# Optimization experiments

Hardware: AMD Instinct MI355X
Metric: run time of the kernel (lower is better)

## Reference

```python
import jax, jax.numpy as jnp
import numpy as np
import math

D_MODEL = 1024
NUM_HEADS = 16
HEAD_DIM = D_MODEL // NUM_HEADS


def _xavier(key, out_f, in_f):
    limit = math.sqrt(6.0 / (in_f + out_f))
    return jax.random.uniform(key, (out_f, in_f), jnp.float32, -limit, limit)


def ternarize(w):
    # abs-mean threshold -> {-1, 0, +1}
    abs_mean = jnp.mean(jnp.abs(w))
    return jnp.where(jnp.abs(w) > abs_mean, jnp.sign(w), jnp.zeros_like(w))


def setup_inputs() -> dict:
    key = jax.random.key(0)
    kq, kk, kv, kwq, kwk, kwv, kwo = jax.random.split(key, 7)
    B, S = 2, 2048
    return {
        "query": jax.random.normal(kq, (B, S, D_MODEL), jnp.float32),
        "key": jax.random.normal(kk, (B, S, D_MODEL), jnp.float32),
        "value": jax.random.normal(kv, (B, S, D_MODEL), jnp.float32),
        "w_q": _xavier(kwq, D_MODEL, D_MODEL),
        "w_k": _xavier(kwk, D_MODEL, D_MODEL),
        "w_v": _xavier(kwv, D_MODEL, D_MODEL),
        "w_o": _xavier(kwo, D_MODEL, D_MODEL),
    }


def reference(query, key, value, w_q, w_k, w_v, w_o):
    B, S, _ = query.shape
    # ternary projections (F.linear: x @ W.T)
    q = query @ ternarize(w_q).T
    k = key @ ternarize(w_k).T
    v = value @ ternarize(w_v).T
    # [B, H, S, Dh]
    q = q.reshape(B, S, NUM_HEADS, HEAD_DIM).transpose(0, 2, 1, 3)
    k = k.reshape(B, -1, NUM_HEADS, HEAD_DIM).transpose(0, 2, 1, 3)
    v = v.reshape(B, -1, NUM_HEADS, HEAD_DIM).transpose(0, 2, 1, 3)
    scores = jnp.einsum("bhqd,bhkd->bhqk", q, k) / math.sqrt(HEAD_DIM)
    probs = jax.nn.softmax(scores, axis=-1)
    out = jnp.einsum("bhqk,bhkd->bhqd", probs, v)
    out = out.transpose(0, 2, 1, 3).reshape(B, S, D_MODEL)
    return out @ ternarize(w_o).T
```

## Files before the change

kernel.cpp:

```cpp
#include <hip/hip_runtime.h>
#include <cstdint>
#include <cstddef>

typedef __bf16 bfloat;
typedef __bf16 bf16x8 __attribute__((ext_vector_type(8)));
typedef __bf16 bf16x4 __attribute__((ext_vector_type(4)));
typedef float  f32x4  __attribute__((ext_vector_type(4)));

static constexpr int D  = 1024;
static constexpr int S  = 2048;
static constexpr int B  = 2;
static constexpr int H  = 16;
static constexpr int DH = 64;
static constexpr int M  = B * S;
static constexpr int WMAT_N = 1024 * 1024;

#define MFMA_BF16(a, b, c) __builtin_amdgcn_mfma_f32_16x16x32_bf16((a), (b), (c), 0, 0, 0)

__device__ __forceinline__ void gl_lds16(const void* g, void* l) {
  __builtin_amdgcn_global_load_lds(
      (const __attribute__((address_space(1))) void*)g,
      (__attribute__((address_space(3))) void*)l, 16, 0, 0);
}

__global__ void absum_kernel(const float* __restrict__ w0, const float* __restrict__ w1,
                             const float* __restrict__ w2, const float* __restrict__ w3,
                             double* __restrict__ sums) {
  int z = blockIdx.y;
  const float* w = (z == 0) ? w0 : (z == 1) ? w1 : (z == 2) ? w2 : w3;
  const float4* w4 = (const float4*)w;
  double s = 0.0;
  for (int i = blockIdx.x * blockDim.x + threadIdx.x; i < (WMAT_N / 4);
       i += gridDim.x * blockDim.x) {
    float4 v = w4[i];
    s += (double)fabsf(v.x) + (double)fabsf(v.y) + (double)fabsf(v.z) + (double)fabsf(v.w);
  }
  for (int off = 1; off < 64; off <<= 1) s += __shfl_xor(s, off, 64);
  __shared__ double ps[4];
  if ((threadIdx.x & 63) == 0) ps[threadIdx.x >> 6] = s;
  __syncthreads();
  if (threadIdx.x == 0) atomicAdd(&sums[z], ps[0] + ps[1] + ps[2] + ps[3]);
}

__global__ void tern_kernel(const float* __restrict__ w0, const float* __restrict__ w1,
                            const float* __restrict__ w2, const float* __restrict__ w3,
                            bfloat* __restrict__ o0, bfloat* __restrict__ o1,
                            bfloat* __restrict__ o2, bfloat* __restrict__ o3,
                            const double* __restrict__ sums) {
  int z = blockIdx.y;
  const float* w = (z == 0) ? w0 : (z == 1) ? w1 : (z == 2) ? w2 : w3;
  bfloat* o = (z == 0) ? o0 : (z == 1) ? o1 : (z == 2) ? o2 : o3;
  double thr = sums[z] * (1.0 / (double)WMAT_N);
  const float4* w4 = (const float4*)w;
  for (int i = blockIdx.x * blockDim.x + threadIdx.x; i < (WMAT_N / 4);
       i += gridDim.x * blockDim.x) {
    float4 v = w4[i];
    bf16x4 r;
    r[0] = (bfloat)(((double)fabsf(v.x) > thr) ? (v.x > 0.f ? 1.f : -1.f) : 0.f);
    r[1] = (bfloat)(((double)fabsf(v.y) > thr) ? (v.y > 0.f ? 1.f : -1.f) : 0.f);
    r[2] = (bfloat)(((double)fabsf(v.z) > thr) ? (v.z > 0.f ? 1.f : -1.f) : 0.f);
    r[3] = (bfloat)(((double)fabsf(v.w) > thr) ? (v.w > 0.f ? 1.f : -1.f) : 0.f);
    *(bf16x4*)&o[(size_t)i * 4] = r;
  }
}

__global__ void splitcvt3_kernel(const float* __restrict__ qx, const float* __restrict__ kx,
                                 const float* __restrict__ vx, bfloat* __restrict__ qhi,
                                 bfloat* __restrict__ qlo, bfloat* __restrict__ khi,
                                 bfloat* __restrict__ klo, bfloat* __restrict__ vhi) {
  int z = blockIdx.y;
  const float* x = (z == 0) ? qx : (z == 1) ? kx : vx;
  bfloat* hi = (z == 0) ? qhi : (z == 1) ? khi : vhi;
  bfloat* lo = (z == 0) ? qlo : (z == 1) ? klo : nullptr;
  const int n4 = M * D / 4;
  const float4* x4 = (const float4*)x;
  for (int i = blockIdx.x * blockDim.x + threadIdx.x; i < n4; i += gridDim.x * blockDim.x) {
    float4 v = x4[i];
    bf16x4 h;
    h[0] = (bfloat)v.x; h[1] = (bfloat)v.y; h[2] = (bfloat)v.z; h[3] = (bfloat)v.w;
    *(bf16x4*)&hi[(size_t)i * 4] = h;
    if (z < 2) {
      bf16x4 l;
      l[0] = (bfloat)(v.x - (float)h[0]);
      l[1] = (bfloat)(v.y - (float)h[1]);
      l[2] = (bfloat)(v.z - (float)h[2]);
      l[3] = (bfloat)(v.w - (float)h[3]);
      *(bf16x4*)&lo[(size_t)i * 4] = l;
    }
  }
}

__global__ __launch_bounds__(256) void qkv_gemm(
    const bfloat* __restrict__ xqh, const bfloat* __restrict__ xql,
    const bfloat* __restrict__ xkh, const bfloat* __restrict__ xkl,
    const bfloat* __restrict__ xvh, const bfloat* __restrict__ wqt,
    const bfloat* __restrict__ wkt, const bfloat* __restrict__ wvt,
    bfloat* __restrict__ qmh, bfloat* __restrict__ qml,
    bfloat* __restrict__ kmh, bfloat* __restrict__ kml, bfloat* __restrict__ vtr) {
  constexpr int K = D;
  constexpr int N = D;
  __shared__ __align__(16) bfloat As0[128 * 32];
  __shared__ __align__(16) bfloat As1[128 * 32];
  __shared__ __align__(16) bfloat Ws[128 * 32];

  const int z = blockIdx.z;
  const bfloat *A0, *A1 = nullptr, *Wm;
  bfloat *Oh = nullptr, *Ol = nullptr;
  float scale = 1.f;
  bool split;
  if (z == 0) {
    A0 = xqh; A1 = xql; Wm = wqt; Oh = qmh; Ol = qml;
    scale = 0.18033688f;
    split = true;
  } else if (z == 1) {
    A0 = xkh; A1 = xkl; Wm = wkt; Oh = kmh; Ol = kml; split = true;
  } else {
    A0 = xvh; Wm = wvt; split = false;
  }

  const int t = threadIdx.x;
  const int w = t >> 6, lane = t & 63;
  const int quad = lane >> 4, l16 = lane & 15;
  const int wm = w >> 1, wn = w & 1;
  const int m0 = blockIdx.y * 128, n0 = blockIdx.x * 128;

  f32x4 acc[4][4] = {};

  const int sr = t >> 2;
  const int cp = t & 3;
  const int cla = cp ^ ((sr >> 1) & 3);
  const int clb = cp ^ (((sr + 64) >> 1) & 3);

  const bfloat* pA0a = A0 + (size_t)(m0 + sr) * K + cla * 8;
  const bfloat* pA0b = A0 + (size_t)(m0 + 64 + sr) * K + clb * 8;
  const bfloat* pA1a = split ? A1 + (size_t)(m0 + sr) * K + cla * 8 : nullptr;
  const bfloat* pA1b = split ? A1 + (size_t)(m0 + 64 + sr) * K + clb * 8 : nullptr;
  const bfloat* pWa = Wm + (size_t)(n0 + sr) * K + cla * 8;
  const bfloat* pWb = Wm + (size_t)(n0 + 64 + sr) * K + clb * 8;

  for (int kk = 0; kk < K; kk += 32) {
    gl_lds16(pA0a + kk, As0 + w * 512);
    gl_lds16(pA0b + kk, As0 + 2048 + w * 512);
    if (split) {
      gl_lds16(pA1a + kk, As1 + w * 512);
      gl_lds16(pA1b + kk, As1 + 2048 + w * 512);
    }
    gl_lds16(pWa + kk, Ws + w * 512);
    gl_lds16(pWb + kk, Ws + 2048 + w * 512);
    __syncthreads();

    bf16x8 bfrag[4], afrag[4];
#pragma unroll
    for (int nt = 0; nt < 4; nt++) {
      int r = wn * 64 + nt * 16 + l16;
      bfrag[nt] = *(const bf16x8*)&Ws[r * 32 + ((quad ^ ((r >> 1) & 3)) * 8)];
    }
#pragma unroll
    for (int mt = 0; mt < 4; mt++) {
      int r = wm * 64 + mt * 16 + l16;
      afrag[mt] = *(const bf16x8*)&As0[r * 32 + ((quad ^ ((r >> 1) & 3)) * 8)];
    }
#pragma unroll
    for (int mt = 0; mt < 4; mt++)
#pragma unroll
      for (int nt = 0; nt < 4; nt++)
        acc[mt][nt] = MFMA_BF16(afrag[mt], bfrag[nt], acc[mt][nt]);
    if (split) {
#pragma unroll
      for (int mt = 0; mt < 4; mt++) {
        int r = wm * 64 + mt * 16 + l16;
        afrag[mt] = *(const bf16x8*)&As1[r * 32 + ((quad ^ ((r >> 1) & 3)) * 8)];
      }
#pragma unroll
      for (int mt = 0; mt < 4; mt++)
#pragma unroll
        for (int nt = 0; nt < 4; nt++)
          acc[mt][nt] = MFMA_BF16(afrag[mt], bfrag[nt], acc[mt][nt]);
    }
    __syncthreads();
  }

#pragma unroll
  for (int mt = 0; mt < 4; mt++) {
#pragma unroll
    for (int nt = 0; nt < 4; nt++) {
      const int row = m0 + wm * 64 + mt * 16 + quad * 4;
      const int col = n0 + wn * 64 + nt * 16 + l16;
      if (split) {
#pragma unroll
        for (int rg = 0; rg < 4; rg++) {
          float vv = acc[mt][nt][rg] * scale;
          size_t idx = (size_t)(row + rg) * N + col;
          bfloat hh = (bfloat)vv;
          Oh[idx] = hh;
          Ol[idx] = (bfloat)(vv - (float)hh);
        }
      } else {
        int bb = row >> 11, s = row & (S - 1);
        bf16x4 pk;
#pragma unroll
        for (int rg = 0; rg < 4; rg++) pk[rg] = (bfloat)acc[mt][nt][rg];
        *(bf16x4*)&vtr[(size_t)bb * D * S + (size_t)col * S + s] = pk;
      }
    }
  }
}

__global__ __launch_bounds__(256) void gemm_wo(const bfloat* __restrict__ A,
                                               const bfloat* __restrict__ Wm,
                                               float* __restrict__ Cf) {
  constexpr int K = D;
  constexpr int N = D;
  __shared__ __align__(16) bfloat As[128 * 32];
  __shared__ __align__(16) bfloat Ws[64 * 32];

  const int t = threadIdx.x;
  const int w = t >> 6, lane = t & 63;
  const int quad = lane >> 4, l16 = lane & 15;
  const int wm = w >> 1, wn = w & 1;
  const int m0 = blockIdx.y * 128, n0 = blockIdx.x * 64;

  f32x4 acc[4][2] = {};

  const int sr = t >> 2;
  const int cp = t & 3;
  const int cla = cp ^ ((sr >> 1) & 3);
  const int clb = cp ^ (((sr + 64) >> 1) & 3);
  const bfloat* pAa = A + (size_t)(m0 + sr) * K + cla * 8;
  const bfloat* pAb = A + (size_t)(m0 + 64 + sr) * K + clb * 8;
  const bfloat* pW = Wm + (size_t)(n0 + sr) * K + cla * 8;

  for (int kk = 0; kk < K; kk += 32) {
    gl_lds16(pAa + kk, As + w * 512);
    gl_lds16(pAb + kk, As + 2048 + w * 512);
    gl_lds16(pW + kk, Ws + w * 512);
    __syncthreads();

    bf16x8 bfrag[2], afrag[4];
#pragma unroll
    for (int nt = 0; nt < 2; nt++) {
      int r = wn * 32 + nt * 16 + l16;
      bfrag[nt] = *(const bf16x8*)&Ws[r * 32 + ((quad ^ ((r >> 1) & 3)) * 8)];
    }
#pragma unroll
    for (int mt = 0; mt < 4; mt++) {
      int r = wm * 64 + mt * 16 + l16;
      afrag[mt] = *(const bf16x8*)&As[r * 32 + ((quad ^ ((r >> 1) & 3)) * 8)];
    }
#pragma unroll
    for (int mt = 0; mt < 4; mt++)
#pragma unroll
      for (int nt = 0; nt < 2; nt++)
        acc[mt][nt] = MFMA_BF16(afrag[mt], bfrag[nt], acc[mt][nt]);
    __syncthreads();
  }

#pragma unroll
  for (int mt = 0; mt < 4; mt++) {
#pragma unroll
    for (int nt = 0; nt < 2; nt++) {
      const int row = m0 + wm * 64 + mt * 16 + quad * 4;
      const int col = n0 + wn * 32 + nt * 16 + l16;
#pragma unroll
      for (int rg = 0; rg < 4; rg++) Cf[(size_t)(row + rg) * N + col] = acc[mt][nt][rg];
    }
  }
}

__global__ __launch_bounds__(256) void flash_kernel(
    const bfloat* __restrict__ qh, const bfloat* __restrict__ ql,
    const bfloat* __restrict__ kh, const bfloat* __restrict__ kl,
    const bfloat* __restrict__ vt, bfloat* __restrict__ outp) {
  __shared__ __align__(16) bfloat Kh[64 * 64];
  __shared__ __align__(16) bfloat Kl[64 * 64];
  __shared__ __align__(16) bfloat Vt[64 * 64];
  __shared__ __align__(16) bfloat Pm[64 * 64];

  const int t = threadIdx.x;
  const int w = t >> 6, lane = t & 63;
  const int quad = lane >> 4, l16 = lane & 15;
  const int b = blockIdx.z, h = blockIdx.y;
  const int q0 = blockIdx.x * 64;
  const size_t base = (size_t)b * S * D + (size_t)h * DH;
  const size_t vbase = (size_t)b * D * S + (size_t)h * DH * S;

  const int ssr = lane >> 3;
  const int spc = lane & 7;

  bf16x8 ones;
#pragma unroll
  for (int j = 0; j < 8; j++) ones[j] = (bfloat)1.f;

#pragma unroll
  for (int g = 0; g < 2; g++) {
    int r = w * 16 + g * 8 + ssr;
    int c = spc ^ (r & 7);
    int lo = (w * 16 + g * 8) * 64;
    gl_lds16(qh + base + (size_t)(q0 + r) * D + c * 8, Kh + lo);
    gl_lds16(ql + base + (size_t)(q0 + r) * D + c * 8, Kl + lo);
  }
  __syncthreads();
  bf16x8 qhf[2], qlf[2];
  {
    int row = w * 16 + l16;
#pragma unroll
    for (int s2 = 0; s2 < 2; s2++) {
      qhf[s2] = *(const bf16x8*)&Kh[row * 64 + (((s2 * 4 + quad) ^ (l16 & 7)) * 8)];
      qlf[s2] = *(const bf16x8*)&Kl[row * 64 + (((s2 * 4 + quad) ^ (l16 & 7)) * 8)];
    }
  }
  __syncthreads();

  f32x4 Oa[4] = {};
  f32x4 La = {};
  float m_i = -3.0e38f;

  for (int k0 = 0; k0 < S; k0 += 64) {
#pragma unroll
    for (int g = 0; g < 2; g++) {
      int r = w * 16 + g * 8 + ssr;
      int c = spc ^ (r & 7);
      int lo = (w * 16 + g * 8) * 64;
      gl_lds16(kh + base + (size_t)(k0 + r) * D + c * 8, Kh + lo);
      gl_lds16(kl + base + (size_t)(k0 + r) * D + c * 8, Kl + lo);
      gl_lds16(vt + vbase + (size_t)r * S + k0 + c * 8, Vt + lo);
    }
    __syncthreads();

    f32x4 sf[4];
#pragma unroll
    for (int mt = 0; mt < 4; mt++) {
      f32x4 a = {};
      int krow = mt * 16 + l16;
#pragma unroll
      for (int s2 = 0; s2 < 2; s2++) {
        bf16x8 bh = *(const bf16x8*)&Kh[krow * 64 + (((s2 * 4 + quad) ^ (l16 & 7)) * 8)];
        bf16x8 bl = *(const bf16x8*)&Kl[krow * 64 + (((s2 * 4 + quad) ^ (l16 & 7)) * 8)];
        a = MFMA_BF16(bh, qhf[s2], a);
        a = MFMA_BF16(bl, qhf[s2], a);
        a = MFMA_BF16(bh, qlf[s2], a);
      }
      sf[mt] = a;
    }

    float mm = sf[0][0];
#pragma unroll
    for (int mt = 0; mt < 4; mt++)
#pragma unroll
      for (int rg = 0; rg < 4; rg++) mm = fmaxf(mm, sf[mt][rg]);
    mm = fmaxf(mm, __shfl_xor(mm, 16, 64));
    mm = fmaxf(mm, __shfl_xor(mm, 32, 64));
    if (__ballot(mm > m_i)) {
      float mnew = fmaxf(m_i, mm);
      float alpha = exp2f(m_i - mnew);
      m_i = mnew;
#pragma unroll
      for (int mt = 0; mt < 4; mt++) Oa[mt] *= alpha;
      La *= alpha;
    }
#pragma unroll
    for (int mt = 0; mt < 4; mt++)
#pragma unroll
      for (int rg = 0; rg < 4; rg++) sf[mt][rg] = exp2f(sf[mt][rg] - m_i);

#pragma unroll
    for (int mt = 0; mt < 4; mt++) {
      bf16x4 pk;
#pragma unroll
      for (int rg = 0; rg < 4; rg++) pk[rg] = (bfloat)sf[mt][rg];
      int g16 = (mt * 2 + (quad >> 1)) ^ (l16 & 7);
      *(bf16x4*)&Pm[(w * 16 + l16) * 64 + g16 * 8 + (quad & 1) * 4] = pk;
    }

#pragma unroll
    for (int s2 = 0; s2 < 2; s2++) {
      bf16x8 pb = *(const bf16x8*)&Pm[(w * 16 + l16) * 64 +
                                      (((s2 * 4 + quad) ^ (l16 & 7)) * 8)];
#pragma unroll
      for (int mt = 0; mt < 4; mt++) {
        int vrow = mt * 16 + l16;
        bf16x8 va = *(const bf16x8*)&Vt[vrow * 64 + (((s2 * 4 + quad) ^ (l16 & 7)) * 8)];
        Oa[mt] = MFMA_BF16(va, pb, Oa[mt]);
      }
      La = MFMA_BF16(ones, pb, La);
    }
    __syncthreads();
  }

  float inv = 1.0f / La[0];
  const int qrow = q0 + w * 16 + l16;
#pragma unroll
  for (int mt = 0; mt < 4; mt++) {
    bf16x4 ov;
#pragma unroll
    for (int rg = 0; rg < 4; rg++) ov[rg] = (bfloat)(Oa[mt][rg] * inv);
    *(bf16x4*)&outp[base + (size_t)qrow * D + mt * 16 + quad * 4] = ov;
  }
}

extern "C" void kernel_launch(void* const* d_in, const int* in_sizes, int n_in,
                              void* d_out, int out_size, void* d_ws, size_t ws_size,
                              hipStream_t stream) {
  const float* q_in = (const float*)d_in[0];
  const float* k_in = (const float*)d_in[1];
  const float* v_in = (const float*)d_in[2];
  const float* wq = (const float*)d_in[3];
  const float* wk = (const float*)d_in[4];
  const float* wv = (const float*)d_in[5];
  const float* wo = (const float*)d_in[6];
  float* outp = (float*)d_out;
  char* ws = (char*)d_ws;

  constexpr size_t WBYTES = (size_t)WMAT_N * 2;
  constexpr size_t XBYTES = (size_t)M * D * 2;
  size_t off = 0;
  double* sums = (double*)(ws + off); off += 256;
  bfloat* wqt = (bfloat*)(ws + off); off += WBYTES;
  bfloat* wkt = (bfloat*)(ws + off); off += WBYTES;
  bfloat* wvt = (bfloat*)(ws + off); off += WBYTES;
  bfloat* wot = (bfloat*)(ws + off); off += WBYTES;
  bfloat* xqh = (bfloat*)(ws + off); off += XBYTES;
  bfloat* xql = (bfloat*)(ws + off); off += XBYTES;
  bfloat* xkh = (bfloat*)(ws + off); off += XBYTES;
  bfloat* xkl = (bfloat*)(ws + off); off += XBYTES;
  bfloat* xvh = (bfloat*)(ws + off); off += XBYTES;
  bfloat* qmh = (bfloat*)(ws + off); off += XBYTES;
  bfloat* qml = (bfloat*)(ws + off); off += XBYTES;
  bfloat* kmh = (bfloat*)(ws + off); off += XBYTES;
  bfloat* kml = (bfloat*)(ws + off); off += XBYTES;
  bfloat* vtr = (bfloat*)(ws + off); off += XBYTES;
  bfloat* attn = xqh;

  hipMemsetAsync(sums, 0, 4 * sizeof(double), stream);
  absum_kernel<<<dim3(128, 4), 256, 0, stream>>>(wq, wk, wv, wo, sums);
  tern_kernel<<<dim3(128, 4), 256, 0, stream>>>(wq, wk, wv, wo, wqt, wkt, wvt, wot, sums);
  splitcvt3_kernel<<<dim3(512, 3), 256, 0, stream>>>(q_in, k_in, v_in, xqh, xql, xkh, xkl, xvh);
  qkv_gemm<<<dim3(D / 128, M / 128, 3), 256, 0, stream>>>(
      xqh, xql, xkh, xkl, xvh, wqt, wkt, wvt, qmh, qml, kmh, kml, vtr);
  flash_kernel<<<dim3(S / 64, H, B), 256, 0, stream>>>(qmh, qml, kmh, kml, vtr, attn);
  gemm_wo<<<dim3(D / 64, M / 128), 256, 0, stream>>>(attn, wot, outp);
}
```

Baseline: 299.4 us.

## Merge prep kernels, deepen QKV GEMM K-tile, shrink output GEMM tiles

Folds the weight abs-sum reduction and the fp32-to-bf16 split conversion into one launch, and widens the conversion to 8 elements per thread. The QKV GEMM now stages 64-wide K slices with an XOR swizzle, which halves the number of barrier round trips per tile. The output projection GEMM moves to 64x64 tiles with a launch-bounds hint, giving more blocks for a small problem. The costs are a larger LDS footprint in the QKV GEMM, which may lower occupancy, and less reuse per block in the output GEMM.

```diff
diff --git a/kernel.cpp b/kernel.cpp
--- a/kernel.cpp
+++ b/kernel.cpp
@@ -23,23 +23,51 @@
       (__attribute__((address_space(3))) void*)l, 16, 0, 0);
 }
 
-__global__ void absum_kernel(const float* __restrict__ w0, const float* __restrict__ w1,
-                             const float* __restrict__ w2, const float* __restrict__ w3,
-                             double* __restrict__ sums) {
-  int z = blockIdx.y;
-  const float* w = (z == 0) ? w0 : (z == 1) ? w1 : (z == 2) ? w2 : w3;
-  const float4* w4 = (const float4*)w;
-  double s = 0.0;
-  for (int i = blockIdx.x * blockDim.x + threadIdx.x; i < (WMAT_N / 4);
-       i += gridDim.x * blockDim.x) {
-    float4 v = w4[i];
-    s += (double)fabsf(v.x) + (double)fabsf(v.y) + (double)fabsf(v.z) + (double)fabsf(v.w);
-  }
-  for (int off = 1; off < 64; off <<= 1) s += __shfl_xor(s, off, 64);
-  __shared__ double ps[4];
-  if ((threadIdx.x & 63) == 0) ps[threadIdx.x >> 6] = s;
-  __syncthreads();
-  if (threadIdx.x == 0) atomicAdd(&sums[z], ps[0] + ps[1] + ps[2] + ps[3]);
+__global__ void prep_kernel(const float* __restrict__ w0, const float* __restrict__ w1,
+                            const float* __restrict__ w2, const float* __restrict__ w3,
+                            const float* __restrict__ qx, const float* __restrict__ kx,
+                            const float* __restrict__ vx, bfloat* __restrict__ qhi,
+                            bfloat* __restrict__ qlo, bfloat* __restrict__ khi,
+                            bfloat* __restrict__ klo, bfloat* __restrict__ vhi,
+                            double* __restrict__ sums) {
+  const int y = blockIdx.y;
+  if (y < 4) {
+    const float* w = (y == 0) ? w0 : (y == 1) ? w1 : (y == 2) ? w2 : w3;
+    const float4* w4 = (const float4*)w;
+    double s = 0.0;
+    for (int i = blockIdx.x * blockDim.x + threadIdx.x; i < (WMAT_N / 4);
+         i += gridDim.x * blockDim.x) {
+      float4 v = w4[i];
+      s += (double)fabsf(v.x) + (double)fabsf(v.y) + (double)fabsf(v.z) + (double)fabsf(v.w);
+    }
+    for (int off = 1; off < 64; off <<= 1) s += __shfl_xor(s, off, 64);
+    __shared__ double ps[4];
+    if ((threadIdx.x & 63) == 0) ps[threadIdx.x >> 6] = s;
+    __syncthreads();
+    if (threadIdx.x == 0) atomicAdd(&sums[y], ps[0] + ps[1] + ps[2] + ps[3]);
+  } else {
+    const int z = y - 4;
+    const float* x = (z == 0) ? qx : (z == 1) ? kx : vx;
+    bfloat* hi = (z == 0) ? qhi : (z == 1) ? khi : vhi;
+    bfloat* lo = (z == 0) ? qlo : (z == 1) ? klo : nullptr;
+    const int n8 = M * D / 8;
+    const float4* x4 = (const float4*)x;
+    for (int i = blockIdx.x * blockDim.x + threadIdx.x; i < n8;
+         i += gridDim.x * blockDim.x) {
+      float4 a = x4[2 * i], b = x4[2 * i + 1];
+      float f[8] = {a.x, a.y, a.z, a.w, b.x, b.y, b.z, b.w};
+      bf16x8 h;
+#pragma unroll
+      for (int j = 0; j < 8; j++) h[j] = (bfloat)f[j];
+      *(bf16x8*)&hi[(size_t)i * 8] = h;
+      if (z < 2) {
+        bf16x8 l;
+#pragma unroll
+        for (int j = 0; j < 8; j++) l[j] = (bfloat)(f[j] - (float)h[j]);
+        *(bf16x8*)&lo[(size_t)i * 8] = l;
+      }
+    }
+  }
 }
 
 __global__ void tern_kernel(const float* __restrict__ w0, const float* __restrict__ w1,
@@ -64,32 +92,6 @@
   }
 }
 
-__global__ void splitcvt3_kernel(const float* __restrict__ qx, const float* __restrict__ kx,
-                                 const float* __restrict__ vx, bfloat* __restrict__ qhi,
-                                 bfloat* __restrict__ qlo, bfloat* __restrict__ khi,
-                                 bfloat* __restrict__ klo, bfloat* __restrict__ vhi) {
-  int z = blockIdx.y;
-  const float* x = (z == 0) ? qx : (z == 1) ? kx : vx;
-  bfloat* hi = (z == 0) ? qhi : (z == 1) ? khi : vhi;
-  bfloat* lo = (z == 0) ? qlo : (z == 1) ? klo : nullptr;
-  const int n4 = M * D / 4;
-  const float4* x4 = (const float4*)x;
-  for (int i = blockIdx.x * blockDim.x + threadIdx.x; i < n4; i += gridDim.x * blockDim.x) {
-    float4 v = x4[i];
-    bf16x4 h;
-    h[0] = (bfloat)v.x; h[1] = (bfloat)v.y; h[2] = (bfloat)v.z; h[3] = (bfloat)v.w;
-    *(bf16x4*)&hi[(size_t)i * 4] = h;
-    if (z < 2) {
-      bf16x4 l;
-      l[0] = (bfloat)(v.x - (float)h[0]);
-      l[1] = (bfloat)(v.y - (float)h[1]);
-      l[2] = (bfloat)(v.z - (float)h[2]);
-      l[3] = (bfloat)(v.w - (float)h[3]);
-      *(bf16x4*)&lo[(size_t)i * 4] = l;
-    }
-  }
-}
-
 __global__ __launch_bounds__(256) void qkv_gemm(
     const bfloat* __restrict__ xqh, const bfloat* __restrict__ xql,
     const bfloat* __restrict__ xkh, const bfloat* __restrict__ xkl,
@@ -99,9 +101,9 @@
     bfloat* __restrict__ kmh, bfloat* __restrict__ kml, bfloat* __restrict__ vtr) {
   constexpr int K = D;
   constexpr int N = D;
-  __shared__ __align__(16) bfloat As0[128 * 32];
-  __shared__ __align__(16) bfloat As1[128 * 32];
-  __shared__ __align__(16) bfloat Ws[128 * 32];
+  __shared__ __align__(16) bfloat As0[128 * 64];
+  __shared__ __align__(16) bfloat As1[128 * 64];
+  __shared__ __align__(16) bfloat Ws[128 * 64];
 
   const int z = blockIdx.z;
   const bfloat *A0, *A1 = nullptr, *Wm;
@@ -126,56 +128,51 @@
 
   f32x4 acc[4][4] = {};
 
-  const int sr = t >> 2;
-  const int cp = t & 3;
-  const int cla = cp ^ ((sr >> 1) & 3);
-  const int clb = cp ^ (((sr + 64) >> 1) & 3);
-
-  const bfloat* pA0a = A0 + (size_t)(m0 + sr) * K + cla * 8;
-  const bfloat* pA0b = A0 + (size_t)(m0 + 64 + sr) * K + clb * 8;
-  const bfloat* pA1a = split ? A1 + (size_t)(m0 + sr) * K + cla * 8 : nullptr;
-  const bfloat* pA1b = split ? A1 + (size_t)(m0 + 64 + sr) * K + clb * 8 : nullptr;
-  const bfloat* pWa = Wm + (size_t)(n0 + sr) * K + cla * 8;
-  const bfloat* pWb = Wm + (size_t)(n0 + 64 + sr) * K + clb * 8;
-
-  for (int kk = 0; kk < K; kk += 32) {
-    gl_lds16(pA0a + kk, As0 + w * 512);
-    gl_lds16(pA0b + kk, As0 + 2048 + w * 512);
-    if (split) {
-      gl_lds16(pA1a + kk, As1 + w * 512);
-      gl_lds16(pA1b + kk, As1 + 2048 + w * 512);
-    }
-    gl_lds16(pWa + kk, Ws + w * 512);
-    gl_lds16(pWb + kk, Ws + 2048 + w * 512);
-    __syncthreads();
-
-    bf16x8 bfrag[4], afrag[4];
-#pragma unroll
-    for (int nt = 0; nt < 4; nt++) {
-      int r = wn * 64 + nt * 16 + l16;
-      bfrag[nt] = *(const bf16x8*)&Ws[r * 32 + ((quad ^ ((r >> 1) & 3)) * 8)];
-    }
-#pragma unroll
-    for (int mt = 0; mt < 4; mt++) {
-      int r = wm * 64 + mt * 16 + l16;
-      afrag[mt] = *(const bf16x8*)&As0[r * 32 + ((quad ^ ((r >> 1) & 3)) * 8)];
-    }
-#pragma unroll
-    for (int mt = 0; mt < 4; mt++)
-#pragma unroll
-      for (int nt = 0; nt < 4; nt++)
-        acc[mt][nt] = MFMA_BF16(afrag[mt], bfrag[nt], acc[mt][nt]);
-    if (split) {
+  const int srr = lane >> 3;
+  const int spc = lane & 7;
+
+  for (int kk = 0; kk < K; kk += 64) {
+#pragma unroll
+    for (int g = 0; g < 4; g++) {
+      int row = w * 32 + g * 8 + srr;
+      int cl = spc ^ (row & 7);
+      int lo = (w * 32 + g * 8) * 64;
+      gl_lds16(A0 + (size_t)(m0 + row) * K + kk + cl * 8, As0 + lo);
+      if (split) gl_lds16(A1 + (size_t)(m0 + row) * K + kk + cl * 8, As1 + lo);
+      gl_lds16(Wm + (size_t)(n0 + row) * K + kk + cl * 8, Ws + lo);
+    }
+    __syncthreads();
+
+#pragma unroll
+    for (int kidx = 0; kidx < 2; kidx++) {
+      bf16x8 bfrag[4], afrag[4];
+#pragma unroll
+      for (int nt = 0; nt < 4; nt++) {
+        int r = wn * 64 + nt * 16 + l16;
+        bfrag[nt] = *(const bf16x8*)&Ws[r * 64 + (((kidx * 4 + quad) ^ (r & 7)) * 8)];
+      }
 #pragma unroll
       for (int mt = 0; mt < 4; mt++) {
         int r = wm * 64 + mt * 16 + l16;
-        afrag[mt] = *(const bf16x8*)&As1[r * 32 + ((quad ^ ((r >> 1) & 3)) * 8)];
+        afrag[mt] = *(const bf16x8*)&As0[r * 64 + (((kidx * 4 + quad) ^ (r & 7)) * 8)];
       }
 #pragma unroll
       for (int mt = 0; mt < 4; mt++)
 #pragma unroll
         for (int nt = 0; nt < 4; nt++)
           acc[mt][nt] = MFMA_BF16(afrag[mt], bfrag[nt], acc[mt][nt]);
+      if (split) {
+#pragma unroll
+        for (int mt = 0; mt < 4; mt++) {
+          int r = wm * 64 + mt * 16 + l16;
+          afrag[mt] = *(const bf16x8*)&As1[r * 64 + (((kidx * 4 + quad) ^ (r & 7)) * 8)];
+        }
+#pragma unroll
+        for (int mt = 0; mt < 4; mt++)
+#pragma unroll
+          for (int nt = 0; nt < 4; nt++)
+            acc[mt][nt] = MFMA_BF16(afrag[mt], bfrag[nt], acc[mt][nt]);
+      }
     }
     __syncthreads();
   }
@@ -206,60 +203,55 @@
   }
 }
 
-__global__ __launch_bounds__(256) void gemm_wo(const bfloat* __restrict__ A,
-                                               const bfloat* __restrict__ Wm,
-                                               float* __restrict__ Cf) {
+__global__ __launch_bounds__(256, 4) void gemm_wo(const bfloat* __restrict__ A,
+                                                  const bfloat* __restrict__ Wm,
+                                                  float* __restrict__ Cf) {
   constexpr int K = D;
   constexpr int N = D;
-  __shared__ __align__(16) bfloat As[128 * 32];
+  __shared__ __align__(16) bfloat As[64 * 32];
   __shared__ __align__(16) bfloat Ws[64 * 32];
 
   const int t = threadIdx.x;
   const int w = t >> 6, lane = t & 63;
   const int quad = lane >> 4, l16 = lane & 15;
   const int wm = w >> 1, wn = w & 1;
-  const int m0 = blockIdx.y * 128, n0 = blockIdx.x * 64;
-
-  f32x4 acc[4][2] = {};
-
-  const int sr = t >> 2;
-  const int cp = t & 3;
-  const int cla = cp ^ ((sr >> 1) & 3);
-  const int clb = cp ^ (((sr + 64) >> 1) & 3);
-  const bfloat* pAa = A + (size_t)(m0 + sr) * K + cla * 8;
-  const bfloat* pAb = A + (size_t)(m0 + 64 + sr) * K + clb * 8;
-  const bfloat* pW = Wm + (size_t)(n0 + sr) * K + cla * 8;
+  const int m0 = blockIdx.y * 64, n0 = blockIdx.x * 64;
+
+  f32x4 acc[2][2] = {};
+
+  const int sr = w * 16 + (lane >> 2);
+  const int sc = (lane & 3) ^ ((sr >> 1) & 3);
+
+  const bfloat* pA = A + (size_t)(m0 + sr) * K + sc * 8;
+  const bfloat* pW = Wm + (size_t)(n0 + sr) * K + sc * 8;
+  const int ldso = w * 16 * 32;
 
   for (int kk = 0; kk < K; kk += 32) {
-    gl_lds16(pAa + kk, As + w * 512);
-    gl_lds16(pAb + kk, As + 2048 + w * 512);
-    gl_lds16(pW + kk, Ws + w * 512);
-    __syncthreads();
-
-    bf16x8 bfrag[2], afrag[4];
+    gl_lds16(pA + kk, As + ldso);
+    gl_lds16(pW + kk, Ws + ldso);
+    __syncthreads();
+
+    bf16x8 af[2], bf[2];
+#pragma unroll
+    for (int i = 0; i < 2; i++) {
+      int ar = wm * 32 + i * 16 + l16;
+      af[i] = *(const bf16x8*)&As[ar * 32 + ((quad ^ ((ar >> 1) & 3)) * 8)];
+      int br = wn * 32 + i * 16 + l16;
+      bf[i] = *(const bf16x8*)&Ws[br * 32 + ((quad ^ ((br >> 1) & 3)) * 8)];
+    }
+#pragma unroll
+    for (int mt = 0; mt < 2; mt++)
+#pragma unroll
+      for (int nt = 0; nt < 2; nt++)
+        acc[mt][nt] = MFMA_BF16(af[mt], bf[nt], acc[mt][nt]);
+    __syncthreads();
+  }
+
+#pragma unroll
+  for (int mt = 0; mt < 2; mt++) {
 #pragma unroll
     for (int nt = 0; nt < 2; nt++) {
-      int r = wn * 32 + nt * 16 + l16;
-      bfrag[nt] = *(const bf16x8*)&Ws[r * 32 + ((quad ^ ((r >> 1) & 3)) * 8)];
-    }
-#pragma unroll
-    for (int mt = 0; mt < 4; mt++) {
-      int r = wm * 64 + mt * 16 + l16;
-      afrag[mt] = *(const bf16x8*)&As[r * 32 + ((quad ^ ((r >> 1) & 3)) * 8)];
-    }
-#pragma unroll
-    for (int mt = 0; mt < 4; mt++)
-#pragma unroll
-      for (int nt = 0; nt < 2; nt++)
-        acc[mt][nt] = MFMA_BF16(afrag[mt], bfrag[nt], acc[mt][nt]);
-    __syncthreads();
-  }
-
-#pragma unroll
-  for (int mt = 0; mt < 4; mt++) {
-#pragma unroll
-    for (int nt = 0; nt < 2; nt++) {
-      const int row = m0 + wm * 64 + mt * 16 + quad * 4;
+      const int row = m0 + wm * 32 + mt * 16 + quad * 4;
       const int col = n0 + wn * 32 + nt * 16 + l16;
 #pragma unroll
       for (int rg = 0; rg < 4; rg++) Cf[(size_t)(row + rg) * N + col] = acc[mt][nt][rg];
@@ -432,11 +424,11 @@
   bfloat* attn = xqh;
 
   hipMemsetAsync(sums, 0, 4 * sizeof(double), stream);
-  absum_kernel<<<dim3(128, 4), 256, 0, stream>>>(wq, wk, wv, wo, sums);
+  prep_kernel<<<dim3(256, 7), 256, 0, stream>>>(
+      wq, wk, wv, wo, q_in, k_in, v_in, xqh, xql, xkh, xkl, xvh, sums);
   tern_kernel<<<dim3(128, 4), 256, 0, stream>>>(wq, wk, wv, wo, wqt, wkt, wvt, wot, sums);
-  splitcvt3_kernel<<<dim3(512, 3), 256, 0, stream>>>(q_in, k_in, v_in, xqh, xql, xkh, xkl, xvh);
   qkv_gemm<<<dim3(D / 128, M / 128, 3), 256, 0, stream>>>(
       xqh, xql, xkh, xkl, xvh, wqt, wkt, wvt, qmh, qml, kmh, kml, vtr);
   flash_kernel<<<dim3(S / 64, H, B), 256, 0, stream>>>(qmh, qml, kmh, kml, vtr, attn);
-  gemm_wo<<<dim3(D / 64, M / 128), 256, 0, stream>>>(attn, wot, outp);
-}
+  gemm_wo<<<dim3(D / 64, M / 64), 256, 0, stream>>>(attn, wot, outp);
+}
```

Result: no change. 294.3 us (-1.7%).
